# Performance work log

Measured on AMD Instinct MI355X. Metric: run time of the kernel, lower is better.

The kernel has to match this reference:

```python
import jax, jax.numpy as jnp
import numpy as np

DIM = 1024
N_HEADS = 16
HEAD_DIM = DIM // N_HEADS
B, S = 2, 2048
NEG = -1e9  # additive causal mask value (finite, safe in low precision)


def setup_inputs() -> dict:
    key = jax.random.key(0)
    k_x, k_q, k_k, k_v, k_o = jax.random.split(key, 5)
    x = jax.random.normal(k_x, (B, S, DIM), dtype=jnp.float32)
    # causal additive mask, broadcastable to [B, H, S, S]
    causal = jnp.triu(jnp.ones((S, S), dtype=bool), k=1)
    mask = jnp.where(causal, NEG, 0.0).astype(jnp.float32)[None, None]
    scale = 1.0 / np.sqrt(DIM)
    wq = jax.random.normal(k_q, (DIM, DIM), dtype=jnp.float32) * scale
    wk = jax.random.normal(k_k, (DIM, DIM), dtype=jnp.float32) * scale
    wv = jax.random.normal(k_v, (DIM, DIM), dtype=jnp.float32) * scale
    wo = jax.random.normal(k_o, (DIM, DIM), dtype=jnp.float32) * scale
    return {"x": x, "mask": mask, "wq": wq, "wk": wk, "wv": wv, "wo": wo}


def reference(x, mask, wq, wk, wv, wo):
    bs, seqlen, _ = x.shape
    # nn.Linear(y) = y @ W^T ; weights stored as (out, in)
    q = (x @ wq.T).reshape(bs, seqlen, N_HEADS, HEAD_DIM)
    k = (x @ wk.T).reshape(bs, seqlen, N_HEADS, HEAD_DIM)
    v = (x @ wv.T).reshape(bs, seqlen, N_HEADS, HEAD_DIM)
    # scores: [B, H, S, S] — intentionally materialized, as in the original
    attn = jnp.einsum('bqhd,bkhd->bhqk', q, k) / np.sqrt(HEAD_DIM)
    attn = attn + mask
    attn = jax.nn.softmax(attn, axis=-1)
    out = jnp.einsum('bhqk,bkhd->bqhd', attn, v).reshape(bs, seqlen, DIM)
    return out @ wo.T
```

## Files before the change

kernel.cpp:

```cpp
#include <hip/hip_runtime.h>

typedef __attribute__((ext_vector_type(8))) short bf16x8;
typedef __attribute__((ext_vector_type(4))) float f32x4;
typedef __attribute__((ext_vector_type(16))) float f32x16;
typedef __attribute__((ext_vector_type(4))) unsigned short u16x4;
typedef __attribute__((ext_vector_type(8))) unsigned short u16x8;

#define DIM 1024
#define SEQ 2048
#define NHEAD 16
#define HDIM 64
#define C2 0.18033688011112042f
#define KFIX 8.0f

__device__ __forceinline__ unsigned short f2bf(float f) {
  union { float f; unsigned u; } v; v.f = f;
  unsigned r = v.u + 0x7fffu + ((v.u >> 16) & 1u);
  return (unsigned short)(r >> 16);
}

__device__ __forceinline__ float bf2f(unsigned short s) {
  union { unsigned u; float f; } v; v.u = ((unsigned)s) << 16;
  return v.f;
}

__device__ __forceinline__ void gload_lds16(const void* g, void* l) {
  __builtin_amdgcn_global_load_lds(
      (const __attribute__((address_space(1))) void*)g,
      (__attribute__((address_space(3))) void*)l, 16, 0, 0);
}

__device__ __forceinline__ f32x16 mfma32(bf16x8 a, bf16x8 b, f32x16 c) {
  return __builtin_amdgcn_mfma_f32_32x32x16_bf16(a, b, c, 0, 0, 0);
}

__device__ __forceinline__ unsigned cvtpk(float lo, float hi) {
  unsigned r;
  asm("v_cvt_pk_bf16_f32 %0, %1, %2" : "=v"(r) : "v"(lo), "v"(hi));
  return r;
}

__global__ void f2bf_all(const float* __restrict__ x, const float* __restrict__ wq,
                         const float* __restrict__ wk, const float* __restrict__ wv,
                         const float* __restrict__ wo, unsigned short* __restrict__ xb,
                         unsigned short* __restrict__ wb) {
  int blk = blockIdx.x;
  const float* src;
  unsigned short* dst;
  int rb;
  if (blk < 4096) { src = x; dst = xb; rb = blk; }
  else {
    int w = (blk - 4096) >> 10;
    src = w == 0 ? wq : w == 1 ? wk : w == 2 ? wv : wo;
    dst = wb + (size_t)w * 1048576;
    rb = (blk - 4096) & 1023;
  }
  int i = rb * 256 + threadIdx.x;
  float4 v = ((const float4*)src)[i];
  u16x4 o;
  o[0] = f2bf(v.x); o[1] = f2bf(v.y); o[2] = f2bf(v.z); o[3] = f2bf(v.w);
  ((u16x4*)dst)[i] = o;
}

__global__ __launch_bounds__(256) void gemm3(
    const unsigned short* __restrict__ xb,
    const unsigned short* __restrict__ wb,
    unsigned short* __restrict__ qkv) {
  __shared__ unsigned short As[128 * 64];
  __shared__ unsigned short Bs[128 * 64];
  const int bz = blockIdx.x;
  const unsigned short *A, *B;
  unsigned short* C;
  int m0, n0, ldc;
  if (bz < 512) {
    int w = bz >> 8, idx = bz & 255;
    m0 = (idx >> 3) * 128; n0 = (idx & 7) * 128;
    A = xb; B = wb + w * 1048576; C = qkv + w * 4194304; ldc = 1024;
  } else {
    int idx = bz - 512;
    m0 = (idx & 7) * 128; n0 = (idx >> 3) * 128;
    A = wb + 2 * 1048576; B = xb; C = qkv + 2 * 4194304; ldc = 4096;
  }
  const float cscale = (bz < 256) ? C2 : 1.0f;
  const int tid = threadIdx.x;
  const int wv = tid >> 6, lane = tid & 63;
  const int g = lane >> 4, l16 = lane & 15;
  const int wm = (wv >> 1) * 64, wn = (wv & 1) * 64;
  f32x4 acc[4][4] = {};

  for (int kt = 0; kt < 1024; kt += 64) {
    __syncthreads();
#pragma unroll
    for (int qq = 0; qq < 4; ++qq) {
      int rbase = wv * 32 + qq * 8;
      int r = rbase + (lane >> 3);
      int cs = ((lane & 7) ^ (r & 7)) * 8;
      gload_lds16(A + (long long)(m0 + r) * 1024 + kt + cs, &As[rbase * 64]);
      gload_lds16(B + (long long)(n0 + r) * 1024 + kt + cs, &Bs[rbase * 64]);
    }
    __syncthreads();
#pragma unroll
    for (int ks = 0; ks < 2; ++ks) {
      bf16x8 af[4], bfr[4];
      const int cb = ks * 64 + g * 16;
#pragma unroll
      for (int mf = 0; mf < 4; ++mf) {
        int row = wm + mf * 16 + l16;
        af[mf] = *(const bf16x8*)((const char*)As + row * 128 + (cb ^ ((row & 7) << 4)));
      }
#pragma unroll
      for (int nf = 0; nf < 4; ++nf) {
        int row = wn + nf * 16 + l16;
        bfr[nf] = *(const bf16x8*)((const char*)Bs + row * 128 + (cb ^ ((row & 7) << 4)));
      }
#pragma unroll
      for (int mf = 0; mf < 4; ++mf)
#pragma unroll
        for (int nf = 0; nf < 4; ++nf)
          acc[mf][nf] = __builtin_amdgcn_mfma_f32_16x16x32_bf16(
              af[mf], bfr[nf], acc[mf][nf], 0, 0, 0);
    }
  }

#pragma unroll
  for (int mf = 0; mf < 4; ++mf)
#pragma unroll
    for (int nf = 0; nf < 4; ++nf)
#pragma unroll
      for (int r = 0; r < 4; ++r) {
        long long m = m0 + wm + mf * 16 + g * 4 + r;
        long long n = n0 + wn + nf * 16 + l16;
        C[m * ldc + n] = f2bf(acc[mf][nf][r] * cscale);
      }
}

__global__ __launch_bounds__(256) void gemm_out(
    const unsigned short* __restrict__ A,
    const unsigned short* __restrict__ B,
    float* __restrict__ C) {
  __shared__ unsigned short As[128 * 64];
  __shared__ unsigned short Bs[128 * 64];
  const int tid = threadIdx.x;
  const int wv = tid >> 6, lane = tid & 63;
  const int g = lane >> 4, l16 = lane & 15;
  const int m0 = blockIdx.y * 128, n0 = blockIdx.x * 128;
  const int wm = (wv >> 1) * 64, wn = (wv & 1) * 64;
  f32x4 acc[4][4] = {};

  for (int kt = 0; kt < 1024; kt += 64) {
    __syncthreads();
#pragma unroll
    for (int qq = 0; qq < 4; ++qq) {
      int rbase = wv * 32 + qq * 8;
      int r = rbase + (lane >> 3);
      int cs = ((lane & 7) ^ (r & 7)) * 8;
      gload_lds16(A + (long long)(m0 + r) * 1024 + kt + cs, &As[rbase * 64]);
      gload_lds16(B + (long long)(n0 + r) * 1024 + kt + cs, &Bs[rbase * 64]);
    }
    __syncthreads();
#pragma unroll
    for (int ks = 0; ks < 2; ++ks) {
      bf16x8 af[4], bfr[4];
      const int cb = ks * 64 + g * 16;
#pragma unroll
      for (int mf = 0; mf < 4; ++mf) {
        int row = wm + mf * 16 + l16;
        af[mf] = *(const bf16x8*)((const char*)As + row * 128 + (cb ^ ((row & 7) << 4)));
      }
#pragma unroll
      for (int nf = 0; nf < 4; ++nf) {
        int row = wn + nf * 16 + l16;
        bfr[nf] = *(const bf16x8*)((const char*)Bs + row * 128 + (cb ^ ((row & 7) << 4)));
      }
#pragma unroll
      for (int mf = 0; mf < 4; ++mf)
#pragma unroll
        for (int nf = 0; nf < 4; ++nf)
          acc[mf][nf] = __builtin_amdgcn_mfma_f32_16x16x32_bf16(
              af[mf], bfr[nf], acc[mf][nf], 0, 0, 0);
    }
  }

#pragma unroll
  for (int mf = 0; mf < 4; ++mf)
#pragma unroll
    for (int nf = 0; nf < 4; ++nf)
#pragma unroll
      for (int r = 0; r < 4; ++r) {
        long long m = m0 + wm + mf * 16 + g * 4 + r;
        long long n = n0 + wn + nf * 16 + l16;
        C[m * 1024 + n] = acc[mf][nf][r];
      }
}

__global__ __launch_bounds__(256, 3) void attn_kernel(
    const unsigned short* __restrict__ Qg,
    const unsigned short* __restrict__ Kg,
    const unsigned short* __restrict__ VTg,
    unsigned short* __restrict__ Og,
    unsigned short* __restrict__ pacc,
    float* __restrict__ pml) {
  __shared__ unsigned short Kls[2][4096];
  __shared__ unsigned short Vls[2][4096];

  const int tid = threadIdx.x;
  const int wv = tid >> 6, lane = tid & 63;
  const int l32 = lane & 31, hi = lane >> 5;
  const int h = blockIdx.y, b = blockIdx.z;

  const int i = blockIdx.x;
  int qt, c, cn;
  if (i < 16)      { qt = 15 - (i >> 2); c = i & 3; cn = 4; }
  else if (i < 28) { int j = i - 16; qt = 11 - j / 3; c = j % 3; cn = 3; }
  else if (i < 36) { int j = i - 28; qt = 7 - ((j >> 1)); c = j & 1; cn = 2; }
  else             { qt = 39 - i; c = 0; cn = 1; }

  const int nt = 2 * qt + 2;
  const int t0 = c * 8;
  const int tb = min(t0 + 8, nt);
  const int tw = min(tb, 2 * qt + (wv >> 1) + 1);

  const int q = qt * 128 + wv * 32 + l32;
  const long long bh = (long long)b * SEQ * DIM + h * HDIM;
  const long long vbase = (long long)h * HDIM * 4096 + b * SEQ;

  const unsigned short* Qrow = Qg + (long long)(b * SEQ + q) * DIM + h * HDIM;
  bf16x8 qf[4];
#pragma unroll
  for (int ds = 0; ds < 4; ++ds)
    qf[ds] = *(const bf16x8*)(Qrow + ds * 16 + hi * 8);

  f32x16 acc0 = {}, acc1 = {};
  float l_run = 0.f;

  const int sr = lane >> 3, sc = lane & 7;
#define STAGE(T, BUF)                                                          \
  {                                                                            \
    const int kv0s = (T) * 64;                                                 \
    _Pragma("unroll")                                                          \
    for (int s = 0; s < 2; ++s) {                                              \
      int jj = wv * 2 + s;                                                     \
      int r = jj * 8 + sr;                                                     \
      int cs = (sc ^ (r & 7)) * 8;                                             \
      gload_lds16(Kg + bh + (long long)(kv0s + r) * DIM + cs,                  \
                  &Kls[BUF][jj * 512]);                                        \
      gload_lds16(VTg + vbase + (long long)r * 4096 + kv0s + cs,               \
                  &Vls[BUF][jj * 512]);                                        \
    }                                                                          \
  }

  STAGE(t0, 0);
  __syncthreads();

  for (int t = t0; t < tb; ++t) {
    const int buf = (t - t0) & 1;
    if (t + 1 < tb) STAGE(t + 1, buf ^ 1);

    if (t < tw) {
      const int kv0 = t * 64;
      f32x16 s0, s1;
#pragma unroll
      for (int r = 0; r < 16; ++r) { s0[r] = -KFIX; s1[r] = -KFIX; }
      __builtin_amdgcn_s_setprio(1);
#pragma unroll
      for (int ds = 0; ds < 4; ++ds) {
        const int cb = (((ds << 1) | hi) ^ (l32 & 7)) * 16;
        bf16x8 k0 = *(const bf16x8*)((const char*)&Kls[buf][0] + l32 * 128 + cb);
        bf16x8 k1 = *(const bf16x8*)((const char*)&Kls[buf][0] + (32 + l32) * 128 + cb);
        s0 = mfma32(k0, qf[ds], s0);
        s1 = mfma32(k1, qf[ds], s1);
      }
      __builtin_amdgcn_s_setprio(0);

      if (kv0 + 64 > q) {
#pragma unroll
        for (int r = 0; r < 16; ++r) {
          int kw = (r & 3) + 8 * (r >> 2) + 4 * hi;
          if (kv0 + kw > q) s0[r] = -1e30f;
          if (kv0 + 32 + kw > q) s1[r] = -1e30f;
        }
      }

      float at[16];
#pragma unroll
      for (int r = 0; r < 16; ++r) {
        float p0 = exp2f(s0[r]);
        float p1 = exp2f(s1[r]);
        s0[r] = p0; s1[r] = p1;
        at[r] = p0 + p1;
      }
#pragma unroll
      for (int off = 8; off; off >>= 1)
#pragma unroll
        for (int i2 = 0; i2 < off; ++i2) at[i2] += at[i2 + off];
      l_run += at[0] + __shfl_xor(at[0], 32);

      __builtin_amdgcn_s_setprio(1);
#pragma unroll
      for (int kks = 0; kks < 4; ++kks) {
        const int base = (kks & 1) * 8;
        unsigned a0, a1, a2, a3;
        if (kks < 2) {
          a0 = cvtpk(s0[base + 0], s0[base + 1]);
          a1 = cvtpk(s0[base + 2], s0[base + 3]);
          a2 = cvtpk(s0[base + 4], s0[base + 5]);
          a3 = cvtpk(s0[base + 6], s0[base + 7]);
        } else {
          a0 = cvtpk(s1[base + 0], s1[base + 1]);
          a1 = cvtpk(s1[base + 2], s1[base + 3]);
          a2 = cvtpk(s1[base + 4], s1[base + 5]);
          a3 = cvtpk(s1[base + 6], s1[base + 7]);
        }
        asm("v_permlane32_swap_b32 %0, %1" : "+v"(a0), "+v"(a2));
        asm("v_permlane32_swap_b32 %0, %1" : "+v"(a1), "+v"(a3));
        union { unsigned u[4]; bf16x8 v; } pf;
        pf.u[0] = a0; pf.u[1] = a1; pf.u[2] = a2; pf.u[3] = a3;
        const int cb = (((kks << 1) | hi) ^ (l32 & 7)) * 16;
        bf16x8 v0 = *(const bf16x8*)((const char*)&Vls[buf][0] + l32 * 128 + cb);
        bf16x8 v1 = *(const bf16x8*)((const char*)&Vls[buf][0] + (32 + l32) * 128 + cb);
        acc0 = mfma32(v0, pf.v, acc0);
        acc1 = mfma32(v1, pf.v, acc1);
      }
      __builtin_amdgcn_s_setprio(0);
    }
    __syncthreads();
  }

  if (cn == 1) {
    const float inv_l = 1.0f / l_run;
    unsigned short* Orow = Og + (long long)(b * SEQ + q) * DIM + h * HDIM;
#pragma unroll
    for (int dblk = 0; dblk < 2; ++dblk) {
#pragma unroll
      for (int g4 = 0; g4 < 4; ++g4) {
        u16x4 o;
#pragma unroll
        for (int jv = 0; jv < 4; ++jv) {
          float v = (dblk ? acc1[g4 * 4 + jv] : acc0[g4 * 4 + jv]) * inv_l;
          o[jv] = f2bf(v);
        }
        *(u16x4*)(Orow + dblk * 32 + 8 * g4 + 4 * hi) = o;
      }
    }
  } else {
    const int sbase = qt < 8 ? 2 * (qt - 4) : qt < 12 ? 8 + 3 * (qt - 8) : 20 + 4 * (qt - 12);
    const int slot = (b * NHEAD + h) * 36 + sbase + c;
    unsigned short* pbase = pacc + (size_t)slot * 8192 + (wv * 32 + l32) * 64;
#pragma unroll
    for (int dblk = 0; dblk < 2; ++dblk) {
#pragma unroll
      for (int g4 = 0; g4 < 4; ++g4) {
        u16x4 o;
#pragma unroll
        for (int jv = 0; jv < 4; ++jv)
          o[jv] = f2bf(dblk ? acc1[g4 * 4 + jv] : acc0[g4 * 4 + jv]);
        *(u16x4*)(pbase + dblk * 32 + 8 * g4 + 4 * hi) = o;
      }
    }
    if (hi == 0) pml[slot * 128 + wv * 32 + l32] = l_run;
  }
}

__global__ __launch_bounds__(256) void attn_merge(
    const unsigned short* __restrict__ pacc,
    const float* __restrict__ pml,
    unsigned short* __restrict__ Og) {
  const int qt = 4 + blockIdx.x;
  const int h = blockIdx.y, b = blockIdx.z;
  const int cn = (qt >> 2) + 1;
  const int sbase = qt < 8 ? 2 * (qt - 4) : qt < 12 ? 8 + 3 * (qt - 8) : 20 + 4 * (qt - 12);
  const int base_slot = (b * NHEAD + h) * 36 + sbase;
  const int t = threadIdx.x;
  const int ql = t >> 1, d0 = (t & 1) * 32;

  float L = 0.f;
#pragma unroll
  for (int cc = 0; cc < 4; ++cc)
    if (cc < cn) L += pml[(base_slot + cc) * 128 + ql];
  const float invL = 1.0f / L;

  float o[32] = {};
#pragma unroll
  for (int cc = 0; cc < 4; ++cc)
    if (cc < cn) {
      const unsigned short* p = pacc + (size_t)(base_slot + cc) * 8192 + ql * 64 + d0;
#pragma unroll
      for (int k = 0; k < 32; k += 8) {
        u16x8 v = *(const u16x8*)(p + k);
#pragma unroll
        for (int jv = 0; jv < 8; ++jv) o[k + jv] += bf2f(v[jv]);
      }
    }

  const int q = qt * 128 + ql;
  unsigned short* orow = Og + (size_t)(b * SEQ + q) * DIM + h * HDIM + d0;
#pragma unroll
  for (int k = 0; k < 32; k += 8) {
    u16x8 ov;
#pragma unroll
    for (int jv = 0; jv < 8; ++jv) ov[jv] = f2bf(o[k + jv] * invL);
    *(u16x8*)(orow + k) = ov;
  }
}

extern "C" void kernel_launch(void* const* d_in, const int* in_sizes, int n_in,
                              void* d_out, int out_size, void* d_ws, size_t ws_size,
                              hipStream_t stream) {
  const float* x   = (const float*)d_in[0];
  const float* wq  = (const float*)d_in[2];
  const float* wk  = (const float*)d_in[3];
  const float* wv_ = (const float*)d_in[4];
  const float* wo  = (const float*)d_in[5];

  unsigned short* xb  = (unsigned short*)d_ws;
  unsigned short* wb  = xb + (size_t)4096 * 1024;
  unsigned short* qkv = wb + (size_t)4 * 1024 * 1024;
  unsigned short* ao  = qkv + (size_t)3 * 4096 * 1024;
  unsigned short* pacc = ao + (size_t)4096 * 1024;
  float* pml = (float*)(pacc + (size_t)1152 * 8192);

  f2bf_all<<<8192, 256, 0, stream>>>(x, wq, wk, wv_, wo, xb, wb);

  gemm3<<<768, 256, 0, stream>>>(xb, wb, qkv);

  attn_kernel<<<dim3(40, 16, 2), 256, 0, stream>>>(
      qkv, qkv + 4194304, qkv + 2 * 4194304, ao, pacc, pml);

  attn_merge<<<dim3(12, 16, 2), 256, 0, stream>>>(pacc, pml, ao);

  gemm_out<<<dim3(8, 32, 1), 256, 0, stream>>>(ao, wb + 3145728, (float*)d_out);
}
```

Measured before the change: 129.0 us.

## Double-buffer LDS tiles in QKV and output GEMMs and remap blocks per XCD

Both projection GEMMs now use two LDS buffers so the global-to-LDS loads for the next K tile are issued while MFMAs run on the current tile, with one barrier per iteration instead of two. The QKV GEMM also remaps block indices so that blocks landing on the same XCD share A rows and L2 locality improves. This doubles LDS per block to 64KB, which may reduce occupancy. Correctness depends on the direct-to-LDS loads having completed before the barrier.

```diff
diff --git a/kernel.cpp b/kernel.cpp
--- a/kernel.cpp
+++ b/kernel.cpp
@@ -66,39 +66,53 @@
     const unsigned short* __restrict__ xb,
     const unsigned short* __restrict__ wb,
     unsigned short* __restrict__ qkv) {
-  __shared__ unsigned short As[128 * 64];
-  __shared__ unsigned short Bs[128 * 64];
+  __shared__ unsigned short As[2][8192];
+  __shared__ unsigned short Bs[2][8192];
   const int bz = blockIdx.x;
   const unsigned short *A, *B;
   unsigned short* C;
   int m0, n0, ldc;
+  float cscale = 1.0f;
   if (bz < 512) {
-    int w = bz >> 8, idx = bz & 255;
-    m0 = (idx >> 3) * 128; n0 = (idx & 7) * 128;
+    int xcd = bz & 7, inner = bz >> 3;
+    int mm = inner & 3, n = (inner >> 2) & 7, w = inner >> 5;
+    m0 = (xcd * 4 + mm) * 128; n0 = n * 128;
     A = xb; B = wb + w * 1048576; C = qkv + w * 4194304; ldc = 1024;
+    if (w == 0) cscale = C2;
   } else {
     int idx = bz - 512;
-    m0 = (idx & 7) * 128; n0 = (idx >> 3) * 128;
+    int xcd = idx & 7, inner = idx >> 3;
+    int tt = inner & 3, mv = inner >> 2;
+    m0 = mv * 128; n0 = (xcd * 4 + tt) * 128;
     A = wb + 2 * 1048576; B = xb; C = qkv + 2 * 4194304; ldc = 4096;
   }
-  const float cscale = (bz < 256) ? C2 : 1.0f;
   const int tid = threadIdx.x;
   const int wv = tid >> 6, lane = tid & 63;
   const int g = lane >> 4, l16 = lane & 15;
   const int wm = (wv >> 1) * 64, wn = (wv & 1) * 64;
   f32x4 acc[4][4] = {};
 
-  for (int kt = 0; kt < 1024; kt += 64) {
-    __syncthreads();
-#pragma unroll
-    for (int qq = 0; qq < 4; ++qq) {
-      int rbase = wv * 32 + qq * 8;
-      int r = rbase + (lane >> 3);
-      int cs = ((lane & 7) ^ (r & 7)) * 8;
-      gload_lds16(A + (long long)(m0 + r) * 1024 + kt + cs, &As[rbase * 64]);
-      gload_lds16(B + (long long)(n0 + r) * 1024 + kt + cs, &Bs[rbase * 64]);
-    }
-    __syncthreads();
+#define GSTAGE(IT, BUF)                                                        \
+  {                                                                            \
+    const int kt = (IT) * 64;                                                  \
+    _Pragma("unroll")                                                          \
+    for (int qq = 0; qq < 4; ++qq) {                                           \
+      int rbase = wv * 32 + qq * 8;                                            \
+      int r = rbase + (lane >> 3);                                             \
+      int cs = ((lane & 7) ^ (r & 7)) * 8;                                     \
+      gload_lds16(A + (long long)(m0 + r) * 1024 + kt + cs,                    \
+                  &As[BUF][rbase * 64]);                                       \
+      gload_lds16(B + (long long)(n0 + r) * 1024 + kt + cs,                    \
+                  &Bs[BUF][rbase * 64]);                                       \
+    }                                                                          \
+  }
+
+  GSTAGE(0, 0);
+  __syncthreads();
+
+  for (int it = 0; it < 16; ++it) {
+    const int buf = it & 1;
+    if (it + 1 < 16) GSTAGE(it + 1, buf ^ 1);
 #pragma unroll
     for (int ks = 0; ks < 2; ++ks) {
       bf16x8 af[4], bfr[4];
@@ -106,12 +120,12 @@
 #pragma unroll
       for (int mf = 0; mf < 4; ++mf) {
         int row = wm + mf * 16 + l16;
-        af[mf] = *(const bf16x8*)((const char*)As + row * 128 + (cb ^ ((row & 7) << 4)));
+        af[mf] = *(const bf16x8*)((const char*)&As[buf][0] + row * 128 + (cb ^ ((row & 7) << 4)));
       }
 #pragma unroll
       for (int nf = 0; nf < 4; ++nf) {
         int row = wn + nf * 16 + l16;
-        bfr[nf] = *(const bf16x8*)((const char*)Bs + row * 128 + (cb ^ ((row & 7) << 4)));
+        bfr[nf] = *(const bf16x8*)((const char*)&Bs[buf][0] + row * 128 + (cb ^ ((row & 7) << 4)));
       }
 #pragma unroll
       for (int mf = 0; mf < 4; ++mf)
@@ -120,6 +134,7 @@
           acc[mf][nf] = __builtin_amdgcn_mfma_f32_16x16x32_bf16(
               af[mf], bfr[nf], acc[mf][nf], 0, 0, 0);
     }
+    __syncthreads();
   }
 
 #pragma unroll
@@ -138,8 +153,8 @@
     const unsigned short* __restrict__ A,
     const unsigned short* __restrict__ B,
     float* __restrict__ C) {
-  __shared__ unsigned short As[128 * 64];
-  __shared__ unsigned short Bs[128 * 64];
+  __shared__ unsigned short As[2][8192];
+  __shared__ unsigned short Bs[2][8192];
   const int tid = threadIdx.x;
   const int wv = tid >> 6, lane = tid & 63;
   const int g = lane >> 4, l16 = lane & 15;
@@ -147,17 +162,27 @@
   const int wm = (wv >> 1) * 64, wn = (wv & 1) * 64;
   f32x4 acc[4][4] = {};
 
-  for (int kt = 0; kt < 1024; kt += 64) {
-    __syncthreads();
-#pragma unroll
-    for (int qq = 0; qq < 4; ++qq) {
-      int rbase = wv * 32 + qq * 8;
-      int r = rbase + (lane >> 3);
-      int cs = ((lane & 7) ^ (r & 7)) * 8;
-      gload_lds16(A + (long long)(m0 + r) * 1024 + kt + cs, &As[rbase * 64]);
-      gload_lds16(B + (long long)(n0 + r) * 1024 + kt + cs, &Bs[rbase * 64]);
-    }
-    __syncthreads();
+#define OSTAGE(IT, BUF)                                                        \
+  {                                                                            \
+    const int kt = (IT) * 64;                                                  \
+    _Pragma("unroll")                                                          \
+    for (int qq = 0; qq < 4; ++qq) {                                           \
+      int rbase = wv * 32 + qq * 8;                                            \
+      int r = rbase + (lane >> 3);                                             \
+      int cs = ((lane & 7) ^ (r & 7)) * 8;                                     \
+      gload_lds16(A + (long long)(m0 + r) * 1024 + kt + cs,                    \
+                  &As[BUF][rbase * 64]);                                       \
+      gload_lds16(B + (long long)(n0 + r) * 1024 + kt + cs,                    \
+                  &Bs[BUF][rbase * 64]);                                       \
+    }                                                                          \
+  }
+
+  OSTAGE(0, 0);
+  __syncthreads();
+
+  for (int it = 0; it < 16; ++it) {
+    const int buf = it & 1;
+    if (it + 1 < 16) OSTAGE(it + 1, buf ^ 1);
 #pragma unroll
     for (int ks = 0; ks < 2; ++ks) {
       bf16x8 af[4], bfr[4];
@@ -165,12 +190,12 @@
 #pragma unroll
       for (int mf = 0; mf < 4; ++mf) {
         int row = wm + mf * 16 + l16;
-        af[mf] = *(const bf16x8*)((const char*)As + row * 128 + (cb ^ ((row & 7) << 4)));
+        af[mf] = *(const bf16x8*)((const char*)&As[buf][0] + row * 128 + (cb ^ ((row & 7) << 4)));
       }
 #pragma unroll
       for (int nf = 0; nf < 4; ++nf) {
         int row = wn + nf * 16 + l16;
-        bfr[nf] = *(const bf16x8*)((const char*)Bs + row * 128 + (cb ^ ((row & 7) << 4)));
+        bfr[nf] = *(const bf16x8*)((const char*)&Bs[buf][0] + row * 128 + (cb ^ ((row & 7) << 4)));
       }
 #pragma unroll
       for (int mf = 0; mf < 4; ++mf)
@@ -179,6 +204,7 @@
           acc[mf][nf] = __builtin_amdgcn_mfma_f32_16x16x32_bf16(
               af[mf], bfr[nf], acc[mf][nf], 0, 0, 0);
     }
+    __syncthreads();
   }
 
 #pragma unroll
```

New measurement: 125.4 us. -2.8%, faster.
